# Kernel optimization log

Hardware: AMD Instinct MI355X
Metric: run time of the kernel (lower is better)

Reference implementation:

```python
import jax, jax.numpy as jnp
import numpy as np

CONF_TH = 0.9
FRACTION = 0.66
IGNORE_INDEX = 255
LAMBDA = 1.0


def setup_inputs() -> dict:
    key = jax.random.key(0)
    pred = jax.random.normal(key, (4, 19, 512, 1024), dtype=jnp.float32)
    return {"pred": pred}


def _image_mask(max_prob, pseudo, num_classes):
    # max_prob, pseudo: [N] flattened per-image. Replicates the torch per-class
    # loop: keep the top floor(count_c * FRACTION) pixels of each class c by
    # max_prob. Equivalent to: within-class descending rank < k_c.
    n = max_prob.shape[0]
    # sort by (class asc, prob desc); last key in lexsort is primary
    order = jnp.lexsort((-max_prob, pseudo))
    counts = jnp.bincount(pseudo, length=num_classes)  # [C]
    starts = jnp.concatenate([jnp.zeros(1, counts.dtype), jnp.cumsum(counts)[:-1]])
    rank_sorted = jnp.arange(n, dtype=counts.dtype) - starts[pseudo[order]]
    rank = jnp.zeros(n, counts.dtype).at[order].set(rank_sorted)
    k = jnp.floor(counts.astype(jnp.float32) * FRACTION).astype(counts.dtype)  # int(count*frac)
    mask_topk = rank < k[pseudo]
    mask_prob = max_prob > CONF_TH
    return mask_prob | mask_topk


def reference(pred):
    B, C, H, W = pred.shape
    logp = jax.nn.log_softmax(pred, axis=1)           # [B,C,H,W]
    prob = jnp.exp(logp)
    pseudo = jnp.argmax(pred, axis=1)                 # [B,H,W] (detached in torch; int here)
    max_prob = jnp.max(prob, axis=1)                  # [B,H,W]
    N = H * W
    mask = jax.vmap(lambda m, p: _image_mask(m, p, C))(
        max_prob.reshape(B, N), pseudo.reshape(B, N)
    ).reshape(B, H, W)
    target = jnp.where(mask, pseudo, IGNORE_INDEX)
    valid = target != IGNORE_INDEX
    tsafe = jnp.where(valid, target, 0)
    nll = -jnp.take_along_axis(logp, tsafe[:, None], axis=1)[:, 0]  # [B,H,W]
    # F.cross_entropy(..., reduction='none') gives 0 at ignored pixels; .mean()
    # divides by the TOTAL number of pixels (including ignored ones).
    loss = jnp.where(valid, nll, 0.0).mean() * LAMBDA
    return loss
```

## Files before the change

### kernel.cpp

```cpp
#include <hip/hip_runtime.h>
#include <math.h>

#define BB 4
#define CC 19
#define NPIX (512 * 1024)
#define NB 80
#define CONF_BIN 72
#define FRACTION_F 0.66f
#define ROW (CC * NB)
#define NROW (BB * CC)

#define NBLK1 512
#define BPI (NBLK1 / BB)
#define PPB (NPIX / BPI)
#define T1 512

typedef float f4 __attribute__((ext_vector_type(4)));


static __device__ __forceinline__ float comp(f4 v, int j) {
    return (j == 0) ? v.x : (j == 1) ? v.y : (j == 2) ? v.z : v.w;
}

__global__ __launch_bounds__(T1, 4) void st_pass1(const float* __restrict__ pred,
                                                  int* __restrict__ cntPart,
                                                  float* __restrict__ snlPart,
                                                  float* __restrict__ out) {
    __shared__ int   hcnt[ROW];
    __shared__ float hsnl[ROW];
    int tid = threadIdx.x;
    if (blockIdx.x == 0 && tid == 0) out[0] = 0.f;
    for (int i = tid; i < ROW; i += T1) { hcnt[i] = 0; hsnl[i] = 0.f; }
    __syncthreads();

    int blk = blockIdx.x;
    int b   = blk >> 7;
    int seg = blk & (BPI - 1);
    const float* bp0 = pred + (size_t)b * CC * NPIX + (size_t)seg * PPB + tid * 4;
    const float* bp1 = bp0 + T1 * 4;

    f4 va[5], vb[5], vc[5], vd[4];
    float m[4], s[4]; int arg[4];

#define LOAD5(DST, BP, C0)                                            \
        _Pragma("unroll")                                             \
        for (int i = 0; i < 5; ++i)                                   \
            DST[i] = __builtin_nontemporal_load((const f4*)((BP) + (size_t)(C0 + i) * NPIX));
#define LOAD4(DST, BP, C0)                                            \
        _Pragma("unroll")                                             \
        for (int i = 0; i < 4; ++i)                                   \
            DST[i] = __builtin_nontemporal_load((const f4*)((BP) + (size_t)(C0 + i) * NPIX));
#define FENCE asm volatile("" ::: "memory")
#define INIT4(VA)                                                     \
        _Pragma("unroll")                                             \
        for (int j = 0; j < 4; ++j) { m[j] = comp(VA[0], j); s[j] = 1.f; arg[j] = 0; }
#define PROC(VA, NCH, CBASE, START)                                   \
        _Pragma("unroll")                                             \
        for (int i = START; i < NCH; ++i) {                           \
            _Pragma("unroll")                                         \
            for (int j = 0; j < 4; ++j) {                             \
                float x  = comp(VA[i], j);                            \
                float nm = fmaxf(m[j], x);                            \
                s[j] = s[j] * __expf(m[j] - nm) + __expf(x - nm);     \
                arg[j] = (x > m[j]) ? (CBASE + i) : arg[j];           \
                m[j] = nm;                                            \
            }                                                         \
        }
#define FINAL()                                                       \
        _Pragma("unroll")                                             \
        for (int j = 0; j < 4; ++j) {                                 \
            float prob = 1.f / s[j];                                  \
            float nll  = __logf(s[j]);                                \
            int bin = min((int)(prob * (float)NB), NB - 1);           \
            int idx = arg[j] * NB + bin;                              \
            atomicAdd(&hcnt[idx], 1);                                 \
            atomicAdd(&hsnl[idx], nll);                               \
        }

    LOAD5(va, bp0, 0); LOAD5(vb, bp0, 5); FENCE;
    INIT4(va)
    PROC(va, 5, 0, 1)
    LOAD5(vc, bp0, 10); FENCE;
    PROC(vb, 5, 5, 0)
    LOAD4(vd, bp0, 15); FENCE;
    PROC(vc, 5, 10, 0)
    LOAD5(va, bp1, 0); FENCE;
    PROC(vd, 4, 15, 0)
    FINAL()
    LOAD5(vb, bp1, 5); FENCE;
    INIT4(va)
    PROC(va, 5, 0, 1)
    LOAD5(vc, bp1, 10); FENCE;
    PROC(vb, 5, 5, 0)
    LOAD4(vd, bp1, 15); FENCE;
    PROC(vc, 5, 10, 0)
    PROC(vd, 4, 15, 0)
    FINAL()
#undef LOAD5
#undef LOAD4
#undef FENCE
#undef INIT4
#undef PROC
#undef FINAL
    __syncthreads();

    int*   cp = cntPart + (size_t)blk * ROW;
    float* sp = snlPart + (size_t)blk * ROW;
    for (int i = tid; i < ROW; i += T1) { cp[i] = hcnt[i]; sp[i] = hsnl[i]; }
}

__global__ __launch_bounds__(384) void st_pass2(const int* __restrict__ cntPart,
                                                const float* __restrict__ snlPart,
                                                float* __restrict__ out) {
    __shared__ int   pcnt[4][NB];
    __shared__ float psnl[4][NB];
    __shared__ int   scnt[NB];
    __shared__ float ssnl[NB];
    int r = blockIdx.x;
    int b = r / CC, c = r - b * CC;
    int tid = threadIdx.x;

    if (tid < 4 * NB) {
        int q   = tid / NB;
        int bin = tid - q * NB;
        size_t off = (size_t)(b * BPI + q * 32) * ROW + (size_t)(c * NB + bin);
        int cs0 = 0, cs1 = 0; float ss0 = 0.f, ss1 = 0.f;
        #pragma unroll 8
        for (int p = 0; p < 32; p += 2) {
            cs0 += cntPart[off + (size_t)p * ROW];
            cs1 += cntPart[off + (size_t)(p + 1) * ROW];
            ss0 += snlPart[off + (size_t)p * ROW];
            ss1 += snlPart[off + (size_t)(p + 1) * ROW];
        }
        pcnt[q][bin] = cs0 + cs1;
        psnl[q][bin] = ss0 + ss1;
    }
    __syncthreads();
    if (tid < NB) {
        scnt[tid] = (pcnt[0][tid] + pcnt[1][tid]) + (pcnt[2][tid] + pcnt[3][tid]);
        ssnl[tid] = (psnl[0][tid] + psnl[1][tid]) + (psnl[2][tid] + psnl[3][tid]);
    }
    __syncthreads();

    if (tid == 0) {
        int count = 0;
        #pragma unroll 8
        for (int i = 0; i < NB; ++i) count += scnt[i];
        float conf = 0.f;
        #pragma unroll 8
        for (int i = CONF_BIN; i < NB; ++i) conf += ssnl[i];
        int k = (int)floorf((float)count * FRACTION_F);
        float sel;
        if (k == 0) {
            sel = conf;
        } else {
            int cum = 0;
            float csum = 0.f;
            int bin = NB - 1;
            int hh = 0;
            for (; bin >= 0; --bin) {
                hh = scnt[bin];
                if (cum + hh >= k) break;
                cum += hh;
                csum += ssnl[bin];
            }
            if (bin < 0) {
                sel = csum;
            } else if (bin >= CONF_BIN) {
                sel = conf;
            } else {
                float avg = ssnl[bin] / (float)max(hh, 1);
                sel = csum + (float)(k - cum) * avg;
            }
        }
        atomicAdd(out, sel * (1.0f / (float)(BB * (size_t)NPIX)));
    }
}

extern "C" void kernel_launch(void* const* d_in, const int* in_sizes, int n_in,
                              void* d_out, int out_size, void* d_ws, size_t ws_size,
                              hipStream_t stream) {
    const float* pred = (const float*)d_in[0];
    float* out = (float*)d_out;

    char* ws = (char*)d_ws;
    int*   cntPart = (int*)ws;
    float* snlPart = (float*)(ws + (size_t)NBLK1 * ROW * sizeof(int));

    st_pass1<<<NBLK1, T1, 0, stream>>>(pred, cntPart, snlPart, out);
    st_pass2<<<NROW, 384, 0, stream>>>(cntPart, snlPart, out);
}
```

Measured before the change: 43.58 us.

## Switch pass1 to float2 loads with full-channel double-buffered pixel groups

Pass 1 now has each thread load float2 vectors across all 19 channels at once, for four 1024-pixel groups, instead of float4 loads staged in chunks of five channels. Two full-channel register buffers alternate so loads for the next group overlap compute on the current one. It also drops the nontemporal load hint. The intent is more memory parallelism per thread and a simpler schedule, at the cost of narrower loads, more load instructions and higher register pressure from the 38 float2 buffers.

```diff
diff --git a/kernel.cpp b/kernel.cpp
--- a/kernel.cpp
+++ b/kernel.cpp
@@ -15,12 +15,8 @@
 #define PPB (NPIX / BPI)
 #define T1 512
 
-typedef float f4 __attribute__((ext_vector_type(4)));
+typedef float f2 __attribute__((ext_vector_type(2)));
 
-
-static __device__ __forceinline__ float comp(f4 v, int j) {
-    return (j == 0) ? v.x : (j == 1) ? v.y : (j == 2) ? v.z : v.w;
-}
 
 __global__ __launch_bounds__(T1, 4) void st_pass1(const float* __restrict__ pred,
                                                   int* __restrict__ cntPart,
@@ -36,72 +32,49 @@
     int blk = blockIdx.x;
     int b   = blk >> 7;
     int seg = blk & (BPI - 1);
-    const float* bp0 = pred + (size_t)b * CC * NPIX + (size_t)seg * PPB + tid * 4;
-    const float* bp1 = bp0 + T1 * 4;
+    const float* base = pred + (size_t)b * CC * NPIX + (size_t)seg * PPB + tid * 2;
 
-    f4 va[5], vb[5], vc[5], vd[4];
-    float m[4], s[4]; int arg[4];
+    f2 A[CC], Bv[CC];
+    float m0, m1, s0, s1; int g0, g1;
 
-#define LOAD5(DST, BP, C0)                                            \
-        _Pragma("unroll")                                             \
-        for (int i = 0; i < 5; ++i)                                   \
-            DST[i] = __builtin_nontemporal_load((const f4*)((BP) + (size_t)(C0 + i) * NPIX));
-#define LOAD4(DST, BP, C0)                                            \
-        _Pragma("unroll")                                             \
-        for (int i = 0; i < 4; ++i)                                   \
-            DST[i] = __builtin_nontemporal_load((const f4*)((BP) + (size_t)(C0 + i) * NPIX));
 #define FENCE asm volatile("" ::: "memory")
-#define INIT4(VA)                                                     \
-        _Pragma("unroll")                                             \
-        for (int j = 0; j < 4; ++j) { m[j] = comp(VA[0], j); s[j] = 1.f; arg[j] = 0; }
-#define PROC(VA, NCH, CBASE, START)                                   \
-        _Pragma("unroll")                                             \
-        for (int i = START; i < NCH; ++i) {                           \
-            _Pragma("unroll")                                         \
-            for (int j = 0; j < 4; ++j) {                             \
-                float x  = comp(VA[i], j);                            \
-                float nm = fmaxf(m[j], x);                            \
-                s[j] = s[j] * __expf(m[j] - nm) + __expf(x - nm);     \
-                arg[j] = (x > m[j]) ? (CBASE + i) : arg[j];           \
-                m[j] = nm;                                            \
-            }                                                         \
-        }
-#define FINAL()                                                       \
-        _Pragma("unroll")                                             \
-        for (int j = 0; j < 4; ++j) {                                 \
-            float prob = 1.f / s[j];                                  \
-            float nll  = __logf(s[j]);                                \
-            int bin = min((int)(prob * (float)NB), NB - 1);           \
-            int idx = arg[j] * NB + bin;                              \
-            atomicAdd(&hcnt[idx], 1);                                 \
-            atomicAdd(&hsnl[idx], nll);                               \
+#define LOADG(BUF, T)                                                  \
+        _Pragma("unroll")                                              \
+        for (int c = 0; c < CC; ++c)                                   \
+            BUF[c] = *(const f2*)(base + (size_t)(T) * 1024 + (size_t)c * NPIX);
+#define COMPUTE(BUF)                                                   \
+        m0 = BUF[0].x; m1 = BUF[0].y; s0 = 1.f; s1 = 1.f; g0 = 0; g1 = 0; \
+        _Pragma("unroll")                                              \
+        for (int c = 1; c < CC; ++c) {                                 \
+            float x0 = BUF[c].x, x1 = BUF[c].y;                        \
+            float n0 = fmaxf(m0, x0), n1 = fmaxf(m1, x1);              \
+            s0 = s0 * __expf(m0 - n0) + __expf(x0 - n0);               \
+            s1 = s1 * __expf(m1 - n1) + __expf(x1 - n1);               \
+            g0 = (x0 > m0) ? c : g0;  g1 = (x1 > m1) ? c : g1;         \
+            m0 = n0; m1 = n1;                                          \
+        }                                                              \
+        {                                                              \
+            float p0 = 1.f / s0, p1 = 1.f / s1;                        \
+            float l0 = __logf(s0), l1 = __logf(s1);                    \
+            int b0 = min((int)(p0 * (float)NB), NB - 1);               \
+            int b1 = min((int)(p1 * (float)NB), NB - 1);               \
+            atomicAdd(&hcnt[g0 * NB + b0], 1);                         \
+            atomicAdd(&hsnl[g0 * NB + b0], l0);                        \
+            atomicAdd(&hcnt[g1 * NB + b1], 1);                         \
+            atomicAdd(&hsnl[g1 * NB + b1], l1);                        \
         }
 
-    LOAD5(va, bp0, 0); LOAD5(vb, bp0, 5); FENCE;
-    INIT4(va)
-    PROC(va, 5, 0, 1)
-    LOAD5(vc, bp0, 10); FENCE;
-    PROC(vb, 5, 5, 0)
-    LOAD4(vd, bp0, 15); FENCE;
-    PROC(vc, 5, 10, 0)
-    LOAD5(va, bp1, 0); FENCE;
-    PROC(vd, 4, 15, 0)
-    FINAL()
-    LOAD5(vb, bp1, 5); FENCE;
-    INIT4(va)
-    PROC(va, 5, 0, 1)
-    LOAD5(vc, bp1, 10); FENCE;
-    PROC(vb, 5, 5, 0)
-    LOAD4(vd, bp1, 15); FENCE;
-    PROC(vc, 5, 10, 0)
-    PROC(vd, 4, 15, 0)
-    FINAL()
-#undef LOAD5
-#undef LOAD4
+    LOADG(A, 0)
+    LOADG(Bv, 1) FENCE;
+    COMPUTE(A)
+    LOADG(A, 2) FENCE;
+    COMPUTE(Bv)
+    LOADG(Bv, 3) FENCE;
+    COMPUTE(A)
+    COMPUTE(Bv)
 #undef FENCE
-#undef INIT4
-#undef PROC
-#undef FINAL
+#undef LOADG
+#undef COMPUTE
     __syncthreads();
 
     int*   cp = cntPart + (size_t)blk * ROW;
```

Result: slower. 58.99 us (+35.3%).
